# Performance work log

Hardware: AMD Instinct MI355X
Metric: run time of the kernel (lower is better)

## Reference

```python
import jax, jax.numpy as jnp
import numpy as np

NUM_VIEW = 300
PHI = (np.sqrt(5.0) - 1.0) / 2.0  # golden-ratio spiral constant


def generate_grasp_views(n):
    # Fibonacci-sphere view sampling (matches graspnet generate_grasp_views)
    i = np.arange(n, dtype=np.float64)
    zi = (2.0 * i + 1.0) / n - 1.0
    r = np.sqrt(np.clip(1.0 - zi * zi, 0.0, None))
    xi = r * np.cos(2.0 * i * np.pi * PHI)
    yi = r * np.sin(2.0 * i * np.pi * PHI)
    return jnp.asarray(np.stack([xi, yi, zi], axis=-1).astype(np.float32))  # [V,3]


def batch_viewpoint_params_to_matrix(towards, angle):
    # towards: [N,3], angle: [N] -> rotation matrices [N,3,3]
    ax = towards
    zeros = jnp.zeros_like(ax[:, 0])
    ay = jnp.stack([-ax[:, 1], ax[:, 0], zeros], axis=-1)
    degenerate = jnp.sum(ay * ay, axis=-1, keepdims=True) == 0
    ay = jnp.where(degenerate, jnp.asarray([0.0, 1.0, 0.0], ax.dtype), ay)
    ax = ax / jnp.linalg.norm(ax, axis=-1, keepdims=True)
    ay = ay / jnp.linalg.norm(ay, axis=-1, keepdims=True)
    az = jnp.cross(ax, ay)
    s, c = jnp.sin(angle), jnp.cos(angle)
    one = jnp.ones_like(s)
    zero = jnp.zeros_like(s)
    R1 = jnp.stack([one, zero, zero, zero, c, -s, zero, s, c], axis=-1).reshape(-1, 3, 3)
    R2 = jnp.stack([ax, ay, az], axis=-1)  # columns are axes
    return jnp.matmul(R2, R1)


def setup_inputs() -> dict:
    key = jax.random.key(0)
    k1, k2 = jax.random.split(key)
    B, N, S = 8, 500000, 4096
    cloud_normals = jax.random.normal(k1, (B, N, 3), dtype=jnp.float32)
    xyz_graspable_idxs = jax.random.randint(k2, (B, S), 0, N, dtype=jnp.int32)
    return {"cloud_normals": cloud_normals, "xyz_graspable_idxs": xyz_graspable_idxs}


def reference(cloud_normals, xyz_graspable_idxs):
    B, S = xyz_graspable_idxs.shape
    # gather_operation: index selected seed normals -> [B, S, 3]
    vp_xyz = jnp.take_along_axis(cloud_normals, xyz_graspable_idxs[..., None].astype(jnp.int32), axis=1)
    views = generate_grasp_views(NUM_VIEW)  # [V,3]
    # brute-force 1-NN over view codebook (squared L2, matches knn_points K=1)
    d2 = (jnp.sum(vp_xyz * vp_xyz, axis=-1, keepdims=True)
          - 2.0 * jnp.einsum("bsd,vd->bsv", vp_xyz, views)
          + jnp.sum(views * views, axis=-1))  # [B,S,V]
    top_view_inds = jnp.argmin(d2, axis=-1)[..., None].astype(jnp.int64)  # [B,S,1]
    # rotation matrices from -normal direction with zero in-plane angle
    flat = (-vp_xyz).reshape(-1, 3)
    angle = jnp.zeros(flat.shape[0], dtype=vp_xyz.dtype)
    vp_rot = batch_viewpoint_params_to_matrix(flat, angle).reshape(B, S, 3, 3)
    return top_view_inds, vp_xyz, vp_rot
```

## Files before the change

kernel.cpp:

```cpp
#include <hip/hip_runtime.h>
#include <math.h>

#define NUM_VIEW 300
#define BSZ 256

#define BB 8
#define NN 500000
#define SS 4096

__global__ __launch_bounds__(BSZ) void normal_policy_kernel(
    const float* __restrict__ cloud_normals,
    const int*   __restrict__ idxs,
    float*       __restrict__ out)
{
    __shared__ float sv[NUM_VIEW][4];
    const double PHI = (sqrt(5.0) - 1.0) / 2.0;
    for (int v = threadIdx.x; v < NUM_VIEW; v += BSZ) {
        double i  = (double)v;
        double zi = (2.0 * i + 1.0) / (double)NUM_VIEW - 1.0;
        double rr = 1.0 - zi * zi;
        if (rr < 0.0) rr = 0.0;
        double r  = sqrt(rr);
        double a  = 2.0 * i * M_PI * PHI;
        float xf = (float)(r * cos(a));
        float yf = (float)(r * sin(a));
        float zf = (float)zi;
        sv[v][0] = xf;
        sv[v][1] = yf;
        sv[v][2] = zf;
        sv[v][3] = (float)((double)xf * xf + (double)yf * yf + (double)zf * zf);
    }
    __syncthreads();

    const int total = BB * SS;
    int p = blockIdx.x * BSZ + threadIdx.x;
    if (p >= total) return;
    int b = p >> 12;
    int idx = idxs[p];
    const float* nptr = cloud_normals + ((size_t)b * NN + (size_t)idx) * 3;
    float nx = nptr[0], ny = nptr[1], nz = nptr[2];

    double dx = (double)nx, dy = (double)ny, dz = (double)nz;
    double xx = dx * dx + dy * dy + dz * dz;
    double best = 1.0e300;
    int bi = 0;
    #pragma unroll 4
    for (int v = 0; v < NUM_VIEW; ++v) {
        double vx = (double)sv[v][0];
        double vy = (double)sv[v][1];
        double vz = (double)sv[v][2];
        double vv = (double)sv[v][3];
        double d2 = xx - 2.0 * (dx * vx + dy * vy + dz * vz) + vv;
        if (d2 < best) { best = d2; bi = v; }
    }

    double axx = -dx, axy = -dy, axz = -dz;
    double ayx = dy, ayy = -dx, ayz = 0.0;
    if (ayx == 0.0 && ayy == 0.0) { ayx = 0.0; ayy = 1.0; ayz = 0.0; }
    double na = sqrt(axx * axx + axy * axy + axz * axz);
    axx /= na; axy /= na; axz /= na;
    double nb = sqrt(ayx * ayx + ayy * ayy + ayz * ayz);
    ayx /= nb; ayy /= nb; ayz /= nb;
    double azx = axy * ayz - axz * ayy;
    double azy = axz * ayx - axx * ayz;
    double azz = axx * ayy - axy * ayx;

    out[p] = (float)bi;
    float* o_xyz = out + total;
    o_xyz[3 * p + 0] = nx;
    o_xyz[3 * p + 1] = ny;
    o_xyz[3 * p + 2] = nz;
    float* o_rot = out + total * 4;
    o_rot[9 * p + 0] = (float)axx;
    o_rot[9 * p + 1] = (float)ayx;
    o_rot[9 * p + 2] = (float)azx;
    o_rot[9 * p + 3] = (float)axy;
    o_rot[9 * p + 4] = (float)ayy;
    o_rot[9 * p + 5] = (float)azy;
    o_rot[9 * p + 6] = (float)axz;
    o_rot[9 * p + 7] = (float)ayz;
    o_rot[9 * p + 8] = (float)azz;
}

extern "C" void kernel_launch(void* const* d_in, const int* in_sizes, int n_in,
                              void* d_out, int out_size, void* d_ws, size_t ws_size,
                              hipStream_t stream) {
    const float* cloud_normals = (const float*)d_in[0];
    const int*   idxs          = (const int*)d_in[1];
    float*       out           = (float*)d_out;
    const int total = BB * SS;
    const int blocks = (total + BSZ - 1) / BSZ;
    hipLaunchKernelGGL(normal_policy_kernel, dim3(blocks), dim3(BSZ), 0, stream,
                       cloud_normals, idxs, out);
}
```

Before: 92.40 us.

## Split view search across four lanes per point and precompute codebook once

Moves the view-codebook generation, with its double-precision trig, into a separate one-block kernel that writes to workspace, so each main block only copies it into shared memory. The main kernel now gives each point four lanes that each scan a quarter of the 300 views and combine their results with xor-shuffles, breaking ties by lower index. Only lane 0 computes and writes the rotation outputs. This raises parallelism on the FP64-heavy search loop, at the cost of an extra launch, four times as many threads doing the redundant gather, and partially idle lanes during the stores.

```diff
diff --git a/kernel.cpp b/kernel.cpp
--- a/kernel.cpp
+++ b/kernel.cpp
@@ -7,35 +7,45 @@
 #define BB 8
 #define NN 500000
 #define SS 4096
+#define TOTAL (BB * SS)
+#define LANES_PER_PT 4
+#define VIEWS_PER_LANE 75
+
+__global__ __launch_bounds__(320) void codebook_kernel(float4* __restrict__ cb) {
+    int v = threadIdx.x;
+    if (v >= NUM_VIEW) return;
+    const double PHI = (sqrt(5.0) - 1.0) / 2.0;
+    double i  = (double)v;
+    double zi = (2.0 * i + 1.0) / (double)NUM_VIEW - 1.0;
+    double rr = 1.0 - zi * zi;
+    if (rr < 0.0) rr = 0.0;
+    double r  = sqrt(rr);
+    double a  = 2.0 * i * M_PI * PHI;
+    float xf = (float)(r * cos(a));
+    float yf = (float)(r * sin(a));
+    float zf = (float)zi;
+    float vv = (float)((double)xf * xf + (double)yf * yf + (double)zf * zf);
+    cb[v] = make_float4(xf, yf, zf, vv);
+}
 
 __global__ __launch_bounds__(BSZ) void normal_policy_kernel(
     const float* __restrict__ cloud_normals,
     const int*   __restrict__ idxs,
+    const float4* __restrict__ cb,
     float*       __restrict__ out)
 {
     __shared__ float sv[NUM_VIEW][4];
-    const double PHI = (sqrt(5.0) - 1.0) / 2.0;
     for (int v = threadIdx.x; v < NUM_VIEW; v += BSZ) {
-        double i  = (double)v;
-        double zi = (2.0 * i + 1.0) / (double)NUM_VIEW - 1.0;
-        double rr = 1.0 - zi * zi;
-        if (rr < 0.0) rr = 0.0;
-        double r  = sqrt(rr);
-        double a  = 2.0 * i * M_PI * PHI;
-        float xf = (float)(r * cos(a));
-        float yf = (float)(r * sin(a));
-        float zf = (float)zi;
-        sv[v][0] = xf;
-        sv[v][1] = yf;
-        sv[v][2] = zf;
-        sv[v][3] = (float)((double)xf * xf + (double)yf * yf + (double)zf * zf);
+        float4 c = cb[v];
+        sv[v][0] = c.x; sv[v][1] = c.y; sv[v][2] = c.z; sv[v][3] = c.w;
     }
     __syncthreads();
 
-    const int total = BB * SS;
-    int p = blockIdx.x * BSZ + threadIdx.x;
-    if (p >= total) return;
+    int t = blockIdx.x * BSZ + threadIdx.x;
+    int p = t >> 2;
+    int r = t & 3;
     int b = p >> 12;
+
     int idx = idxs[p];
     const float* nptr = cloud_normals + ((size_t)b * NN + (size_t)idx) * 3;
     float nx = nptr[0], ny = nptr[1], nz = nptr[2];
@@ -44,8 +54,10 @@
     double xx = dx * dx + dy * dy + dz * dz;
     double best = 1.0e300;
     int bi = 0;
-    #pragma unroll 4
-    for (int v = 0; v < NUM_VIEW; ++v) {
+    int vbase = r * VIEWS_PER_LANE;
+    #pragma unroll 5
+    for (int j = 0; j < VIEWS_PER_LANE; ++j) {
+        int v = vbase + j;
         double vx = (double)sv[v][0];
         double vy = (double)sv[v][1];
         double vz = (double)sv[v][2];
@@ -54,32 +66,41 @@
         if (d2 < best) { best = d2; bi = v; }
     }
 
-    double axx = -dx, axy = -dy, axz = -dz;
-    double ayx = dy, ayy = -dx, ayz = 0.0;
-    if (ayx == 0.0 && ayy == 0.0) { ayx = 0.0; ayy = 1.0; ayz = 0.0; }
-    double na = sqrt(axx * axx + axy * axy + axz * axz);
-    axx /= na; axy /= na; axz /= na;
-    double nb = sqrt(ayx * ayx + ayy * ayy + ayz * ayz);
-    ayx /= nb; ayy /= nb; ayz /= nb;
-    double azx = axy * ayz - axz * ayy;
-    double azy = axz * ayx - axx * ayz;
-    double azz = axx * ayy - axy * ayx;
+    #pragma unroll
+    for (int m = 1; m <= 2; m <<= 1) {
+        double ob = __shfl_xor(best, m, 64);
+        int    oi = __shfl_xor(bi,   m, 64);
+        if (ob < best || (ob == best && oi < bi)) { best = ob; bi = oi; }
+    }
 
-    out[p] = (float)bi;
-    float* o_xyz = out + total;
-    o_xyz[3 * p + 0] = nx;
-    o_xyz[3 * p + 1] = ny;
-    o_xyz[3 * p + 2] = nz;
-    float* o_rot = out + total * 4;
-    o_rot[9 * p + 0] = (float)axx;
-    o_rot[9 * p + 1] = (float)ayx;
-    o_rot[9 * p + 2] = (float)azx;
-    o_rot[9 * p + 3] = (float)axy;
-    o_rot[9 * p + 4] = (float)ayy;
-    o_rot[9 * p + 5] = (float)azy;
-    o_rot[9 * p + 6] = (float)axz;
-    o_rot[9 * p + 7] = (float)ayz;
-    o_rot[9 * p + 8] = (float)azz;
+    if (r == 0) {
+        double axx = -dx, axy = -dy, axz = -dz;
+        double ayx = dy, ayy = -dx, ayz = 0.0;
+        if (ayx == 0.0 && ayy == 0.0) { ayx = 0.0; ayy = 1.0; ayz = 0.0; }
+        double ia = 1.0 / sqrt(axx * axx + axy * axy + axz * axz);
+        axx *= ia; axy *= ia; axz *= ia;
+        double ib = 1.0 / sqrt(ayx * ayx + ayy * ayy + ayz * ayz);
+        ayx *= ib; ayy *= ib; ayz *= ib;
+        double azx = axy * ayz - axz * ayy;
+        double azy = axz * ayx - axx * ayz;
+        double azz = axx * ayy - axy * ayx;
+
+        out[p] = (float)bi;
+        float* o_xyz = out + TOTAL;
+        o_xyz[3 * p + 0] = nx;
+        o_xyz[3 * p + 1] = ny;
+        o_xyz[3 * p + 2] = nz;
+        float* o_rot = out + TOTAL * 4;
+        o_rot[9 * p + 0] = (float)axx;
+        o_rot[9 * p + 1] = (float)ayx;
+        o_rot[9 * p + 2] = (float)azx;
+        o_rot[9 * p + 3] = (float)axy;
+        o_rot[9 * p + 4] = (float)ayy;
+        o_rot[9 * p + 5] = (float)azy;
+        o_rot[9 * p + 6] = (float)axz;
+        o_rot[9 * p + 7] = (float)ayz;
+        o_rot[9 * p + 8] = (float)azz;
+    }
 }
 
 extern "C" void kernel_launch(void* const* d_in, const int* in_sizes, int n_in,
@@ -88,8 +109,12 @@
     const float* cloud_normals = (const float*)d_in[0];
     const int*   idxs          = (const int*)d_in[1];
     float*       out           = (float*)d_out;
-    const int total = BB * SS;
-    const int blocks = (total + BSZ - 1) / BSZ;
+    float4*      cb            = (float4*)d_ws;
+
+    hipLaunchKernelGGL(codebook_kernel, dim3(1), dim3(320), 0, stream, cb);
+
+    const int threads = TOTAL * LANES_PER_PT;
+    const int blocks  = threads / BSZ;
     hipLaunchKernelGGL(normal_policy_kernel, dim3(blocks), dim3(BSZ), 0, stream,
-                       cloud_normals, idxs, out);
+                       cloud_normals, idxs, cb, out);
 }
```

After: 85.76 us. 7.2% less time.
